# Optimization experiments

Hardware: AMD Instinct MI355X
Metric: run time of the kernel (lower is better)

The kernel has to match this reference:

```python
import jax, jax.numpy as jnp
import numpy as np

IN_CH = 256
SCALES = (128.0, 256.0, 512.0)
RATIOS = (0.5, 1.0, 2.0)
A = len(SCALES) * len(RATIOS)
PRE_NMS_TOPK = 2000
POST_NMS_TOPK = 1000
NMS_IOU = 0.7
MIN_SIZE = 16.0
RPN_BATCH = 256
POS_FRAC = 0.5
BBOX_CLAMP = float(np.log(1000.0 / 16.0))


def conv2d(x, w, b, pad):
    y = jax.lax.conv_general_dilated(x, w, (1, 1), [(pad, pad), (pad, pad)],
                                     dimension_numbers=('NCHW', 'OIHW', 'NCHW'))
    return y + b[None, :, None, None]


def generate_anchors(img_hw, feat_hw):
    H, W = img_hw
    Hf, Wf = feat_hw
    sh, sw = H // Hf, W // Wf
    r = jnp.asarray(RATIOS, jnp.float32)
    s = jnp.asarray(SCALES, jnp.float32)
    hr = jnp.sqrt(r)
    wr = 1.0 / hr
    ws = (wr[:, None] * s[None, :]).reshape(-1)  # [A]
    hs = (hr[:, None] * s[None, :]).reshape(-1)
    base = jnp.stack([-ws, -hs, ws, hs], axis=1) * 0.5  # [A,4] zero-centered
    xs = jnp.arange(Wf, dtype=jnp.float32) * sw
    ys = jnp.arange(Hf, dtype=jnp.float32) * sh
    yy, xx = jnp.meshgrid(ys, xs, indexing='ij')
    shifts = jnp.stack([xx, yy, xx, yy], axis=-1).reshape(-1, 4)  # [Hf*Wf,4]
    return (shifts[:, None, :] + base[None, :, :]).reshape(-1, 4)  # [Hf*Wf*A,4]


def apply_deltas(anchors, deltas):
    aw = anchors[:, 2] - anchors[:, 0]
    ah = anchors[:, 3] - anchors[:, 1]
    acx = anchors[:, 0] + 0.5 * aw
    acy = anchors[:, 1] + 0.5 * ah
    dx, dy = deltas[:, 0], deltas[:, 1]
    dw = jnp.minimum(deltas[:, 2], BBOX_CLAMP)
    dh = jnp.minimum(deltas[:, 3], BBOX_CLAMP)
    cx = dx * aw + acx
    cy = dy * ah + acy
    w = jnp.exp(dw) * aw
    h = jnp.exp(dh) * ah
    return jnp.stack([cx - 0.5 * w, cy - 0.5 * h, cx + 0.5 * w, cy + 0.5 * h], axis=1)


def boxes_to_deltas(boxes, anchors):
    aw = anchors[:, 2] - anchors[:, 0]
    ah = anchors[:, 3] - anchors[:, 1]
    acx = anchors[:, 0] + 0.5 * aw
    acy = anchors[:, 1] + 0.5 * ah
    gw = boxes[:, 2] - boxes[:, 0]
    gh = boxes[:, 3] - boxes[:, 1]
    gcx = boxes[:, 0] + 0.5 * gw
    gcy = boxes[:, 1] + 0.5 * gh
    return jnp.stack([(gcx - acx) / aw, (gcy - acy) / ah,
                      jnp.log(gw / aw), jnp.log(gh / ah)], axis=1)


def iou_matrix(a, b):
    area_a = (a[:, 2] - a[:, 0]) * (a[:, 3] - a[:, 1])
    area_b = (b[:, 2] - b[:, 0]) * (b[:, 3] - b[:, 1])
    lt = jnp.maximum(a[:, None, :2], b[None, :, :2])
    rb = jnp.minimum(a[:, None, 2:], b[None, :, 2:])
    wh = jnp.clip(rb - lt, 0.0)
    inter = wh[..., 0] * wh[..., 1]
    return inter / (area_a[:, None] + area_b[None, :] - inter)


def filter_proposals(proposals, logits):
    k = PRE_NMS_TOPK
    top_scores, idx = jax.lax.top_k(logits, k)
    boxes = proposals[idx]
    probs = jax.nn.sigmoid(top_scores)
    bw = boxes[:, 2] - boxes[:, 0]
    bh = boxes[:, 3] - boxes[:, 1]
    probs = jnp.where((bw >= MIN_SIZE) & (bh >= MIN_SIZE), probs, -jnp.inf)
    order = jnp.argsort(-probs)
    boxes = boxes[order]
    probs = probs[order]
    iou = iou_matrix(boxes, boxes)  # [k,k]
    idxs = jnp.arange(k)

    def body(i, keep):
        suppress = keep[i] & (iou[i] > NMS_IOU) & (idxs > i)
        return keep & ~suppress

    keep = jax.lax.fori_loop(0, k, body, jnp.ones(k, bool))
    kept = jnp.where(keep, probs, -jnp.inf)
    final_scores, fidx = jax.lax.top_k(kept, POST_NMS_TOPK)
    return boxes[fidx], final_scores


def _forward(image, feat_map, gt_boxes, w_rpn, b_rpn, w_reg, b_reg, w_cls, b_cls):
    img_hw = image.shape[-2:]
    feat_hw = feat_map.shape[-2:]
    conv_out = jax.nn.relu(conv2d(feat_map, w_rpn, b_rpn, 1))
    reg = conv2d(conv_out, w_reg, b_reg, 0).transpose(0, 2, 3, 1).reshape(-1, 4)
    cls = conv2d(conv_out, w_cls, b_cls, 0).transpose(0, 2, 3, 1).reshape(-1)
    anchors = generate_anchors(img_hw, feat_hw)  # [N,4]
    proposals = apply_deltas(anchors, jax.lax.stop_gradient(reg))
    H, W = img_hw
    proposals = jnp.stack([jnp.clip(proposals[:, 0], 0.0, W),
                           jnp.clip(proposals[:, 1], 0.0, H),
                           jnp.clip(proposals[:, 2], 0.0, W),
                           jnp.clip(proposals[:, 3], 0.0, H)], axis=1)
    prop_out, score_out = filter_proposals(proposals, jax.lax.stop_gradient(cls))

    # --- target assignment (training path) ---
    gt = gt_boxes[0]  # [M,4]
    iou = iou_matrix(anchors, gt)  # [N,M]
    max_iou = iou.max(axis=1)
    argmax_gt = iou.argmax(axis=1)
    labels = jnp.where(max_iou >= 0.7, 1.0, jnp.where(max_iou < 0.3, 0.0, -1.0))
    best_per_gt = iou.max(axis=0)  # [M]
    force_pos = (iou == best_per_gt[None, :]).any(axis=1)
    labels = jnp.where(force_pos, 1.0, labels)
    matched = gt[argmax_gt]
    tgt_deltas = boxes_to_deltas(matched, anchors)

    # --- deterministic positive/negative sampling (fixed key) ---
    N = labels.shape[0]
    u = jax.random.uniform(jax.random.key(42), (N,))
    pos_cap = int(POS_FRAC * RPN_BATCH)
    pv, pi = jax.lax.top_k(jnp.where(labels == 1.0, u, -jnp.inf), pos_cap)
    pos_valid = pv > -jnp.inf
    pos_mask = jnp.zeros(N, bool).at[pi].set(pos_valid)
    num_pos = pos_valid.sum()
    nv, ni = jax.lax.top_k(jnp.where(labels == 0.0, u, -jnp.inf), RPN_BATCH)
    neg_valid = (nv > -jnp.inf) & (jnp.arange(RPN_BATCH) < (RPN_BATCH - num_pos))
    neg_mask = jnp.zeros(N, bool).at[ni].set(neg_valid)
    samp_mask = pos_mask | neg_mask
    n_samp = samp_mask.sum().astype(jnp.float32)

    # BCE with logits (stable), mean over sampled anchors
    bce = jnp.maximum(cls, 0.0) - cls * labels + jnp.log1p(jnp.exp(-jnp.abs(cls)))
    cls_loss = jnp.sum(jnp.where(samp_mask, bce, 0.0)) / n_samp

    # smooth L1 (beta=1/9), sum over positives / num sampled
    beta = 1.0 / 9.0
    d = reg - tgt_deltas
    ad = jnp.abs(d)
    sl1 = jnp.where(ad < beta, 0.5 * d * d / beta, ad - 0.5 * beta)
    loc_loss = jnp.sum(jnp.where(pos_mask[:, None], sl1, 0.0)) / n_samp

    return prop_out, score_out, cls_loss, loc_loss


def setup_inputs() -> dict:
    key = jax.random.key(0)
    ks = jax.random.split(key, 8)
    image = jax.random.normal(ks[0], (1, 3, 800, 800), jnp.float32)
    feat_map = jax.random.normal(ks[1], (1, IN_CH, 100, 100), jnp.float32)
    cxy = jax.random.uniform(ks[2], (1, 20, 2), minval=100.0, maxval=700.0)
    wh = jax.random.uniform(ks[3], (1, 20, 2), minval=50.0, maxval=300.0)
    gt_boxes = jnp.concatenate([jnp.clip(cxy - 0.5 * wh, 0.0, 800.0),
                                jnp.clip(cxy + 0.5 * wh, 0.0, 800.0)], axis=-1)
    w_rpn = 0.01 * jax.random.normal(ks[4], (IN_CH, IN_CH, 3, 3), jnp.float32)
    b_rpn = jnp.zeros((IN_CH,), jnp.float32)
    w_reg = 0.01 * jax.random.normal(ks[5], (A * 4, IN_CH, 1, 1), jnp.float32)
    b_reg = jnp.zeros((A * 4,), jnp.float32)
    w_cls = 0.01 * jax.random.normal(ks[6], (A, IN_CH, 1, 1), jnp.float32)
    b_cls = jnp.zeros((A,), jnp.float32)
    return dict(image=image, feat_map=feat_map, gt_boxes=gt_boxes,
                w_rpn=w_rpn, b_rpn=b_rpn, w_reg=w_reg, b_reg=b_reg,
                w_cls=w_cls, b_cls=b_cls)


def reference(image, feat_map, gt_boxes, w_rpn, b_rpn, w_reg, b_reg, w_cls, b_cls):
    return _forward(image, feat_map, gt_boxes, w_rpn, b_rpn, w_reg, b_reg, w_cls, b_cls)
```

## Files before the change

### kernel.cpp

```cpp
#include <hip/hip_runtime.h>
#include <cstdint>
#include <cstddef>
#include <math.h>

typedef unsigned int u32;
typedef unsigned long long u64;
typedef unsigned char u8;
typedef signed char i8;
typedef unsigned short u16;

#define NPIX 10000
#define NANCH 90000
#define NGT 20
#define DIVUP(a,b) (((a)+(b)-1)/(b))

static constexpr float BBOX_CLAMP_F = 4.135166556742356f;
static constexpr float BETA_F       = 0.1111111111111111111f;
static constexpr float HALF_BETA_F  = 0.0555555555555555556f;

static constexpr size_t algn(size_t x){ return (x + 255) & ~size_t(255); }
static constexpr size_t OFF_WT   = 0;
static constexpr size_t OFF_W1T  = algn(OFF_WT   + size_t(2304)*256*4);
static constexpr size_t OFF_REG  = algn(OFF_W1T  + size_t(64*48*4)*4);
static constexpr size_t OFF_CLS  = algn(OFF_REG  + size_t(NANCH)*4*4);
static constexpr size_t OFF_PROP = algn(OFF_CLS  + size_t(NANCH)*4);
static constexpr size_t OFF_UB   = algn(OFF_PROP + size_t(NANCH)*4*4);
static constexpr size_t OFF_LAB  = algn(OFF_UB   + size_t(NANCH)*4);
static constexpr size_t OFF_AMX  = algn(OFF_LAB  + NANCH);
static constexpr size_t OFF_BGTP = algn(OFF_AMX  + NANCH);
static constexpr size_t OFF_BGT  = algn(OFF_BGTP + 1280*20*4);
static constexpr size_t OFF_BOXA = algn(OFF_BGT  + 256);
static constexpr size_t OFF_BOX2 = algn(OFF_BOXA + 2048*4*4);
static constexpr size_t OFF_PRB2 = algn(OFF_BOX2 + 2048*4*4);
static constexpr size_t OFF_SPRB = algn(OFF_PRB2 + 2048*4);
static constexpr size_t OFF_MASK = algn(OFF_SPRB + 2048*4);
static constexpr size_t OFF_CAND = algn(OFF_MASK + size_t(2048)*32*8);
static constexpr size_t OFF_CND2 = algn(OFF_CAND + 2048*8);
static constexpr size_t OFF_POSL = algn(OFF_CND2 + 4096*8);
static constexpr size_t OFF_EQN  = algn(OFF_POSL + 4096*4);
static constexpr size_t OFF_KEEP = algn(OFF_EQN  + 1024*8);
static constexpr size_t OFF_Z0   = algn(OFF_KEEP + 32*8);
static constexpr size_t OFF_H0   = OFF_Z0;
static constexpr size_t OFF_H2   = OFF_H0 + 65536*4;
static constexpr size_t OFF_META = OFF_H2 + 65536*4;
static constexpr size_t ZERO_END = OFF_META + 256;
static constexpr int ZERO_WORDS  = int((ZERO_END - OFF_Z0) / 4);

enum { M_CAND_CNT=0, M_POS_CNT, M_EQN_CNT, M_NEED_NEG,
       M_BIN_L_HI, M_CUM_L_HI, M_BIN_N_HI, M_CUM_N_HI,
       M_ACC_CLS, M_ACC_LOC, M_N_SAMP, M_CAND2_CNT };

__device__ __forceinline__ u32 rotl32(u32 x, int d){ return (x<<d)|(x>>(32-d)); }

__device__ __forceinline__ u32 threefry_bits(u32 i) {
  const u32 ks0 = 0u, ks1 = 42u, ks2 = 0x1BD11BDAu ^ 0u ^ 42u;
  u32 x0 = 0u + ks0, x1 = i + ks1;
  x0+=x1; x1=rotl32(x1,13); x1^=x0;
  x0+=x1; x1=rotl32(x1,15); x1^=x0;
  x0+=x1; x1=rotl32(x1,26); x1^=x0;
  x0+=x1; x1=rotl32(x1, 6); x1^=x0;
  x0+=ks1; x1+=ks2+1u;
  x0+=x1; x1=rotl32(x1,17); x1^=x0;
  x0+=x1; x1=rotl32(x1,29); x1^=x0;
  x0+=x1; x1=rotl32(x1,16); x1^=x0;
  x0+=x1; x1=rotl32(x1,24); x1^=x0;
  x0+=ks2; x1+=ks0+2u;
  x0+=x1; x1=rotl32(x1,13); x1^=x0;
  x0+=x1; x1=rotl32(x1,15); x1^=x0;
  x0+=x1; x1=rotl32(x1,26); x1^=x0;
  x0+=x1; x1=rotl32(x1, 6); x1^=x0;
  x0+=ks0; x1+=ks1+3u;
  x0+=x1; x1=rotl32(x1,17); x1^=x0;
  x0+=x1; x1=rotl32(x1,29); x1^=x0;
  x0+=x1; x1=rotl32(x1,16); x1^=x0;
  x0+=x1; x1=rotl32(x1,24); x1^=x0;
  x0+=ks1; x1+=ks2+4u;
  x0+=x1; x1=rotl32(x1,13); x1^=x0;
  x0+=x1; x1=rotl32(x1,15); x1^=x0;
  x0+=x1; x1=rotl32(x1,26); x1^=x0;
  x0+=x1; x1=rotl32(x1, 6); x1^=x0;
  x0+=ks2; x1+=ks0+5u;
  return x1;
}

__device__ __forceinline__ u32 rand_u_bits(u32 i) {
  u32 b = threefry_bits(i);
  float f = __uint_as_float((b >> 9) | 0x3F800000u) - 1.0f;
  return __float_as_uint(f);
}

__device__ __forceinline__ u32 fkey(float x) {
  u32 u = __float_as_uint(x);
  return (u & 0x80000000u) ? ~u : (u | 0x80000000u);
}

__device__ void bitonic_desc(u64* s, int N, int tid, int nthr) {
  for (int k = 2; k <= N; k <<= 1) {
    for (int j = k >> 1; j > 0; j >>= 1) {
      __syncthreads();
      for (int i = tid; i < N; i += nthr) {
        int ixj = i ^ j;
        if (ixj > i) {
          u64 a = s[i], b = s[ixj];
          bool up = ((i & k) == 0);
          if ((a < b) == up) { s[i] = b; s[ixj] = a; }
        }
      }
    }
  }
  __syncthreads();
}

__device__ __forceinline__ int wave_append(u32* cnt, bool pred) {
  u64 mb = __ballot(pred);
  if (mb == 0ull) return -1;
  int lane = threadIdx.x & 63;
  int leader = __ffsll((unsigned long long)mb) - 1;
  u32 base = 0;
  if (lane == leader) base = atomicAdd(cnt, (u32)__popcll(mb));
  base = __shfl(base, leader, 64);
  if (!pred) return -1;
  return (int)(base + (u32)__popcll(mb & ((1ull << lane) - 1ull)));
}

__device__ __forceinline__ u32 group_sum256(const u32* __restrict__ h, int g, int lane) {
  uint4 v = ((const uint4*)(h + (size_t)g*256))[lane];
  u32 s = v.x + v.y + v.z + v.w;
  #pragma unroll
  for (int off = 32; off > 0; off >>= 1) s += __shfl_down(s, off, 64);
  return s;
}

__global__ __launch_bounds__(256) void k_init(const float* __restrict__ w,
                                              const float* __restrict__ w_reg,
                                              const float* __restrict__ w_cls,
                                              float* __restrict__ wT,
                                              float* __restrict__ w1T,
                                              u32* __restrict__ zbase, int zwords) {
  int b = blockIdx.x;
  int t = threadIdx.x;
  if (b < 144) {
    __shared__ float sm[64][65];
    int ct = b / 36, et = b % 36;
    int e0 = et*64, co0 = ct*64;
    int lane = t & 63, rr = t >> 6;
    #pragma unroll
    for (int r4 = 0; r4 < 16; ++r4) {
      int row = r4*4 + rr;
      sm[row][lane] = w[(size_t)(co0+row)*2304 + e0 + lane];
    }
    __syncthreads();
    #pragma unroll
    for (int r4 = 0; r4 < 16; ++r4) {
      int erow = r4*4 + rr;
      wT[(size_t)(e0+erow)*256 + co0 + lane] = sm[lane][erow];
    }
  } else if (b == 144) {
    for (int i = t; i < 64*48*4; i += 256) {
      int e = i & 3, c = (i >> 2) % 48, g = (i >> 2) / 48;
      float v = 0.f;
      if (c < 36) v = w_reg[(size_t)c*256 + g*4 + e];
      else if (c < 45) v = w_cls[(size_t)(c-36)*256 + g*4 + e];
      w1T[i] = v;
    }
  } else {
    int nb = gridDim.x - 145;
    for (int i = (b-145)*256 + t; i < zwords; i += nb*256) zbase[i] = 0u;
  }
}

__device__ __forceinline__ float conv1_dot_t(const float4* __restrict__ f4,
                                             const float4* __restrict__ w1T4,
                                             int c, float bias) {
  float acc = bias;
  #pragma unroll 8
  for (int g = 0; g < 64; ++g) {
    float4 a = f4[g], b = w1T4[g*48 + c];
    acc += a.x*b.x + a.y*b.y + a.z*b.z + a.w*b.w;
  }
  return acc;
}

#pragma clang fp contract(off)

__device__ __forceinline__ void anchor_of(int n, float& a0, float& a1, float& a2, float& a3) {
  int px = n / 9, a = n % 9;
  int y = px / 100, x = px % 100;
  int ri = a / 3, si = a % 3;
  const float R[3] = {0.5f, 1.0f, 2.0f};
  const float S[3] = {128.f, 256.f, 512.f};
  float hr = sqrtf(R[ri]);
  float wr = 1.0f / hr;
  float wsa = wr * S[si], hsa = hr * S[si];
  float sx = (float)x * 8.0f, sy = (float)y * 8.0f;
  a0 = sx + (-wsa) * 0.5f;
  a1 = sy + (-hsa) * 0.5f;
  a2 = sx + wsa * 0.5f;
  a3 = sy + hsa * 0.5f;
}

__device__ __forceinline__ float iou_one(float a0,float a1,float a2,float a3,float aarea,
                                         const float* __restrict__ gt, int g) {
  float g0=gt[g*4+0], g1=gt[g*4+1], g2=gt[g*4+2], g3=gt[g*4+3];
  float garea=(g2-g0)*(g3-g1);
  float ix0=fmaxf(a0,g0), iy0=fmaxf(a1,g1);
  float ix1=fminf(a2,g2), iy1=fminf(a3,g3);
  float iw=fmaxf(ix1-ix0,0.f), ih=fmaxf(iy1-iy0,0.f);
  float inter=iw*ih;
  return inter/(aarea+garea-inter);
}

__device__ __forceinline__ float bce_of(float c, float l) {
  return fmaxf(c,0.f) - c*l + log1pf(expf(-fabsf(c)));
}

__global__ __launch_bounds__(256) void k_conv3(const float* __restrict__ feat,
                                               const float* __restrict__ wT,
                                               const float* __restrict__ bias,
                                               const float* __restrict__ w1T,
                                               const float* __restrict__ b_reg,
                                               const float* __restrict__ b_cls,
                                               const float* __restrict__ gt,
                                               float* __restrict__ reg,
                                               float* __restrict__ cls,
                                               float* __restrict__ prop,
                                               u32* __restrict__ h0,
                                               i8* __restrict__ label,
                                               u8* __restrict__ amax,
                                               u32* __restrict__ ub,
                                               float* __restrict__ bgtp) {
  const int co = threadIdx.x;
  const int y0 = (blockIdx.x / 25) * 2;
  const int x0 = (blockIdx.x % 25) * 4;
  __shared__ __align__(16) float sf[16][4][8];
  __shared__ __align__(16) float sacc[8][256];
  __shared__ float shead[8][48];
  __shared__ float sbias[48];
  __shared__ float sgt[80];
  __shared__ float svm[72][20];
  float acc[2][4];
  #pragma unroll
  for (int r = 0; r < 2; ++r)
    #pragma unroll
    for (int p = 0; p < 4; ++p) acc[r][p] = 0.f;

  for (int cb = 0; cb < 256; cb += 16) {
    __syncthreads();
    #pragma unroll
    for (int e = threadIdx.x; e < 512; e += 256) {
      int ci = e >> 5, rem = e & 31, r = rem >> 3, xx = rem & 7;
      int gy = y0 - 1 + r, gx = x0 - 1 + xx;
      float v = 0.f;
      if ((unsigned)gy < 100u && (unsigned)gx < 100u) v = feat[(cb+ci)*NPIX + gy*100 + gx];
      sf[ci][r][xx] = v;
    }
    __syncthreads();
    float wv0[9], wv1[9];
    {
      const float* wp = wT + (size_t)(cb*9)*256 + co;
      #pragma unroll
      for (int k = 0; k < 9; ++k) wv0[k] = wp[k*256];
    }
    #pragma unroll
    for (int ci = 0; ci < 16; ++ci) {
      float* cur = (ci & 1) ? wv1 : wv0;
      float* nxt = (ci & 1) ? wv0 : wv1;
      if (ci < 15) {
        const float* wp = wT + (size_t)((cb+ci+1)*9)*256 + co;
        #pragma unroll
        for (int k = 0; k < 9; ++k) nxt[k] = wp[k*256];
      }
      #pragma unroll
      for (int ir = 0; ir < 4; ++ir) {
        const float4* rp4 = (const float4*)&sf[ci][ir][0];
        float4 q0 = rp4[0], q1 = rp4[1];
        float rw[6] = {q0.x, q0.y, q0.z, q0.w, q1.x, q1.y};
        #pragma unroll
        for (int ky = 0; ky < 3; ++ky) {
          const int ro = ir - ky;
          if (ro >= 0 && ro < 2) {
            #pragma unroll
            for (int kx = 0; kx < 3; ++kx) {
              const float wvv = cur[ky*3+kx];
              #pragma unroll
              for (int p = 0; p < 4; ++p)
                acc[ro][p] = fmaf(wvv, rw[p+kx], acc[ro][p]);
            }
          }
        }
      }
    }
  }
  float b = bias[co];
  #pragma unroll
  for (int r = 0; r < 2; ++r)
    #pragma unroll
    for (int p = 0; p < 4; ++p)
      sacc[r*4+p][co] = fmaxf(acc[r][p] + b, 0.f);
  if (threadIdx.x < 45)
    sbias[threadIdx.x] = (threadIdx.x < 36) ? b_reg[threadIdx.x] : b_cls[threadIdx.x-36];
  if (threadIdx.x < 80) sgt[threadIdx.x] = gt[threadIdx.x];
  __syncthreads();
  for (int task = threadIdx.x; task < 360; task += 256) {
    int pl = task / 45, c = task % 45;
    float v = conv1_dot_t((const float4*)&sacc[pl][0], (const float4*)w1T, c, sbias[c]);
    shead[pl][c] = v;
    int px = (y0 + (pl >> 2))*100 + x0 + (pl & 3);
    if (c < 36) reg[(size_t)px*36 + c] = v;
    else        cls[(size_t)px*9 + (c-36)] = v;
  }
  __syncthreads();
  if (threadIdx.x < 72) {
    int pl = threadIdx.x / 9, aidx = threadIdx.x % 9;
    int px = (y0 + (pl >> 2))*100 + x0 + (pl & 3);
    int n = px*9 + aidx;
    float a0,a1,a2,a3; anchor_of(n, a0,a1,a2,a3);
    float aw = a2 - a0, ah = a3 - a1;
    float acx = a0 + 0.5f*aw, acy = a1 + 0.5f*ah;
    {
      float dx = shead[pl][aidx*4+0], dy = shead[pl][aidx*4+1];
      float dw = fminf(shead[pl][aidx*4+2], BBOX_CLAMP_F);
      float dh = fminf(shead[pl][aidx*4+3], BBOX_CLAMP_F);
      float lg = shead[pl][36+aidx];
      float cx = dx*aw + acx, cy = dy*ah + acy;
      float w = expf(dw)*aw, h = expf(dh)*ah;
      float p0 = cx - 0.5f*w, p1 = cy - 0.5f*h, p2 = cx + 0.5f*w, p3 = cy + 0.5f*h;
      p0 = fminf(fmaxf(p0, 0.f), 800.f);
      p1 = fminf(fmaxf(p1, 0.f), 800.f);
      p2 = fminf(fmaxf(p2, 0.f), 800.f);
      p3 = fminf(fmaxf(p3, 0.f), 800.f);
      prop[(size_t)n*4+0] = p0; prop[(size_t)n*4+1] = p1;
      prop[(size_t)n*4+2] = p2; prop[(size_t)n*4+3] = p3;
      atomicAdd(&h0[fkey(lg) >> 16], 1u);
    }
    float aarea = (a2-a0)*(a3-a1);
    float best = -1.f; int bg = 0;
    for (int g = 0; g < NGT; ++g) {
      float iou = iou_one(a0,a1,a2,a3,aarea,sgt,g);
      svm[threadIdx.x][g] = iou;
      if (iou > best) { best = iou; bg = g; }
    }
    label[n] = (best >= 0.7f) ? (i8)1 : ((best < 0.3f) ? (i8)0 : (i8)-1);
    amax[n] = (u8)bg;
    ub[n] = rand_u_bits((u32)n);
  }
  __syncthreads();
  if (threadIdx.x < NGT) {
    float m = 0.f;
    for (int r = 0; r < 72; ++r) m = fmaxf(m, svm[r][threadIdx.x]);
    bgtp[(size_t)blockIdx.x*NGT + threadIdx.x] = m;
  }
}

__global__ __launch_bounds__(1024) void k_scan(const u32* __restrict__ h0,
                                               const float* __restrict__ bgtp,
                                               u32* __restrict__ meta,
                                               float* __restrict__ bgt) {
  __shared__ u32 part[256], buf[256], sseg, scum;
  __shared__ float pb[32][20];
  int tid = threadIdx.x;
  int lane = tid & 63, wave = tid >> 6;
  for (int gi = 0; gi < 16; ++gi) {
    int g = wave*16 + gi;
    u32 s = group_sum256(h0, g, lane);
    if (lane == 0) part[g] = s;
  }
  if (tid < 640) {
    int g = tid % 20, ch = tid / 20;
    int r0 = ch*40, r1 = r0 + 40; if (r1 > 1250) r1 = 1250;
    float m = 0.f;
    for (int r = r0; r < r1; ++r) m = fmaxf(m, bgtp[(size_t)r*NGT + g]);
    pb[ch][g] = m;
  }
  __syncthreads();
  if (tid == 0) {
    u32 cum = 0; int seg = 255;
    for (; seg > 0; --seg) { if (cum + part[seg] >= 2000u) break; cum += part[seg]; }
    sseg = (u32)seg; scum = cum;
  }
  if (tid < 20) {
    float m = 0.f;
    #pragma unroll
    for (int c = 0; c < 32; ++c) m = fmaxf(m, pb[c][tid]);
    bgt[tid] = m;
  }
  __syncthreads();
  if (tid < 256) buf[tid] = h0[sseg*256 + tid];
  __syncthreads();
  if (tid == 0) {
    u32 cum = scum; int bin = (int)sseg*256;
    for (int i = 255; i >= 0; --i) {
      u32 h = buf[i];
      if (cum + h >= 2000u) { bin = (int)sseg*256 + i; break; }
      cum += h;
    }
    meta[M_BIN_L_HI] = (u32)bin;
  }
}

__global__ __launch_bounds__(256) void k_force(const float* __restrict__ cls,
                                               const float* __restrict__ bgt,
                                               const float* __restrict__ gt,
                                               i8* __restrict__ label,
                                               const u32* __restrict__ ub,
                                               u32* __restrict__ meta,
                                               u32* __restrict__ poslist,
                                               u32* __restrict__ h2,
                                               u64* __restrict__ cand,
                                               u64* __restrict__ cand2) {
  __shared__ float sgt[80], sbgt[20];
  int tid = threadIdx.x;
  if (tid < 80) sgt[tid] = gt[tid];
  if (tid < 20) sbgt[tid] = bgt[tid];
  __syncthreads();
  int n = blockIdx.x*256 + tid;
  bool valid = n < NANCH;
  u32 bin = meta[M_BIN_L_HI];
  bool pos = false, predA = false, predB = false; u64 ckey = 0;
  if (valid) {
    u32 k = fkey(cls[n]);
    u32 hi = k >> 16;
    if (hi >= bin) {
      ckey = ((u64)k << 32) | (u64)(0xFFFFFFFFu - (u32)n);
      if (hi > bin) predA = true; else predB = true;
    }
    float a0,a1,a2,a3; anchor_of(n, a0,a1,a2,a3);
    float aarea = (a2-a0)*(a3-a1);
    bool force = false;
    for (int g = 0; g < NGT; ++g)
      if (iou_one(a0,a1,a2,a3,aarea,sgt,g) == sbgt[g]) force = true;
    i8 lab = label[n];
    if (force) lab = 1;
    label[n] = lab;
    if (lab == 1) pos = true;
    else if (lab == 0) atomicAdd(&h2[ub[n] >> 16], 1u);
  }
  int slot = wave_append(&meta[M_POS_CNT], pos);
  if (pos && slot >= 0 && slot < 4096) poslist[slot] = (u32)n;
  int aslot = wave_append(&meta[M_CAND_CNT], predA);
  if (predA && aslot >= 0 && aslot < 2048) cand[aslot] = ckey;
  int bslot = wave_append(&meta[M_CAND2_CNT], predB);
  if (predB && bslot >= 0 && bslot < 4096) cand2[bslot] = ckey;
}

struct MidSh {
  union {
    struct { u64 ss[2048]; } srtA;
    struct { u64 ss[4096]; } srtB;
    struct { u32 part[256]; u32 buf[256]; } ns;
    struct { u64 ss[4096]; u32 sel[128]; float red[1024]; } ps;
  } u;
  u32 sseg, scum;
};

__device__ __forceinline__ void mid_gather(const u64* __restrict__ ss, int cnt, int base,
                                           const float* __restrict__ cls,
                                           const float* __restrict__ prop,
                                           float* __restrict__ boxA,
                                           float* __restrict__ sprobG,
                                           int tid) {
  for (int t = tid; t < cnt; t += 1024) {
    int rank = base + t;
    if (rank >= 2000) break;
    u32 n = 0xFFFFFFFFu - (u32)ss[t];
    float b0 = prop[(size_t)n*4+0], b1 = prop[(size_t)n*4+1];
    float b2 = prop[(size_t)n*4+2], b3 = prop[(size_t)n*4+3];
    float logit = cls[n];
    float p = 1.0f / (1.0f + expf(-logit));
    float bw = b2 - b0, bh = b3 - b1;
    if (!(bw >= 16.0f && bh >= 16.0f)) p = -INFINITY;
    boxA[rank*4+0] = b0; boxA[rank*4+1] = b1; boxA[rank*4+2] = b2; boxA[rank*4+3] = b3;
    sprobG[rank] = p;
  }
}

__global__ __launch_bounds__(1024) void k_mid(const u64* __restrict__ cand,
                                              const u64* __restrict__ cand2,
                                              const float* __restrict__ cls,
                                              const float* __restrict__ prop,
                                              const float* __restrict__ reg,
                                              const float* __restrict__ gt,
                                              const u32* __restrict__ ub,
                                              const u32* __restrict__ poslist,
                                              const u8* __restrict__ amax,
                                              const u32* __restrict__ h2,
                                              u32* __restrict__ meta,
                                              float* __restrict__ boxA,
                                              float* __restrict__ sprobG) {
  __shared__ MidSh S;
  int tid = threadIdx.x;
  int lane = tid & 63, wave = tid >> 6;
  if (blockIdx.x == 0) {
    u32 c1 = meta[M_CAND_CNT]; if (c1 > 2048u) c1 = 2048u;
    if (c1 > 0) {
      int N = 256; while (N < (int)c1) N <<= 1;
      for (int i = tid; i < N; i += 1024) S.u.srtA.ss[i] = (i < (int)c1) ? cand[i] : 0ull;
      bitonic_desc(S.u.srtA.ss, N, tid, 1024);
      mid_gather(S.u.srtA.ss, (int)c1, 0, cls, prop, boxA, sprobG, tid);
    }
  } else if (blockIdx.x == 3) {
    u32 c1 = meta[M_CAND_CNT]; if (c1 > 2048u) c1 = 2048u;
    u32 c2 = meta[M_CAND2_CNT]; if (c2 > 4096u) c2 = 4096u;
    int lim = 2000 - (int)c1; if (lim < 0) lim = 0; if (lim > (int)c2) lim = (int)c2;
    if (c2 > 0 && lim > 0) {
      int N = 256; while (N < (int)c2) N <<= 1;
      for (int i = tid; i < N; i += 1024) S.u.srtB.ss[i] = (i < (int)c2) ? cand2[i] : 0ull;
      bitonic_desc(S.u.srtB.ss, N, tid, 1024);
      mid_gather(S.u.srtB.ss, lim, (int)c1, cls, prop, boxA, sprobG, tid);
    }
  } else if (blockIdx.x == 1) {
    u32 pc = meta[M_POS_CNT]; if (pc > 4096u) pc = 4096u;
    int npos = pc < 128u ? (int)pc : 128;
    u32 need = (u32)(256 - npos);
    if (tid == 0) meta[M_NEED_NEG] = need;
    for (int gi = 0; gi < 16; ++gi) {
      int g = wave*16 + gi;
      u32 s = group_sum256(h2, g, lane);
      if (lane == 0) S.u.ns.part[g] = s;
    }
    __syncthreads();
    if (tid == 0) {
      u32 cum = 0; int seg = 255;
      for (; seg > 0; --seg) { if (cum + S.u.ns.part[seg] >= need) break; cum += S.u.ns.part[seg]; }
      S.sseg = (u32)seg; S.scum = cum;
    }
    __syncthreads();
    if (tid < 256) S.u.ns.buf[tid] = h2[S.sseg*256 + tid];
    __syncthreads();
    if (tid == 0) {
      u32 cum = S.scum; int bin = (int)S.sseg*256;
      for (int i = 255; i >= 0; --i) {
        u32 h = S.u.ns.buf[i];
        if (cum + h >= need) { bin = (int)S.sseg*256 + i; break; }
        cum += h;
      }
      meta[M_BIN_N_HI] = (u32)bin;
      meta[M_CUM_N_HI] = cum;
    }
  } else {
    u32 m = meta[M_POS_CNT]; if (m > 4096u) m = 4096u;
    int npos = m < 128u ? (int)m : 128;
    if (m > 128u) {
      int N = 256; while (N < (int)m) N <<= 1;
      for (int i = tid; i < N; i += 1024)
        S.u.ps.ss[i] = (i < (int)m)
          ? (((u64)ub[poslist[i]] << 32) | (u64)(0xFFFFFFFFu - poslist[i]))
          : 0ull;
      bitonic_desc(S.u.ps.ss, N, tid, 1024);
      if (tid < 128) S.u.ps.sel[tid] = 0xFFFFFFFFu - (u32)S.u.ps.ss[tid];
    } else {
      if (tid < (int)m) S.u.ps.sel[tid] = poslist[tid];
    }
    __syncthreads();
    float accC = 0.f, accL = 0.f;
    if (tid < npos) {
      int n = (int)S.u.ps.sel[tid];
      float c = cls[n];
      accC = bce_of(c, 1.0f);
      float a0,a1,a2,a3; anchor_of(n, a0,a1,a2,a3);
      float aw = a2-a0, ah = a3-a1;
      float acx = a0 + 0.5f*aw, acy = a1 + 0.5f*ah;
      int g = amax[n];
      float g0 = gt[g*4+0], g1 = gt[g*4+1], g2 = gt[g*4+2], g3 = gt[g*4+3];
      float gw = g2-g0, gh = g3-g1;
      float gcx = g0 + 0.5f*gw, gcy = g1 + 0.5f*gh;
      float t0 = (gcx-acx)/aw, t1 = (gcy-acy)/ah;
      float t2 = logf(gw/aw), t3 = logf(gh/ah);
      float tt[4] = {t0,t1,t2,t3};
      float sl = 0.f;
      for (int j = 0; j < 4; ++j) {
        float d = reg[(size_t)n*4 + j] - tt[j];
        float ad = fabsf(d);
        sl += (ad < BETA_F) ? (((0.5f*d)*d)/BETA_F) : (ad - HALF_BETA_F);
      }
      accL = sl;
    }
    __syncthreads();
    S.u.ps.red[tid] = accC;
    __syncthreads();
    for (int s = 512; s > 0; s >>= 1) {
      if (tid < s) S.u.ps.red[tid] = S.u.ps.red[tid] + S.u.ps.red[tid+s];
      __syncthreads();
    }
    float totC = S.u.ps.red[0];
    __syncthreads();
    S.u.ps.red[tid] = accL;
    __syncthreads();
    for (int s = 512; s > 0; s >>= 1) {
      if (tid < s) S.u.ps.red[tid] = S.u.ps.red[tid] + S.u.ps.red[tid+s];
      __syncthreads();
    }
    if (tid == 0) {
      float* mf = (float*)meta;
      atomicAdd(&mf[M_ACC_CLS], totC);
      atomicAdd(&mf[M_ACC_LOC], S.u.ps.red[0]);
      atomicAdd(&meta[M_N_SAMP], (u32)npos);
    }
  }
}

struct NnSh {
  union {
    struct { float bx0[2000], by0[2000], bx1[2000], by1[2000], bar[2000], sp[2000];
             u16 dmap[2000]; } nms;
    struct { float redf[1024]; u32 redc[1024]; } neg;
  } u;
};

__global__ __launch_bounds__(1024) void k_nn(const float* __restrict__ boxA,
                                             const float* __restrict__ sprobG,
                                             const float* __restrict__ cls,
                                             const i8* __restrict__ label,
                                             const u32* __restrict__ ub,
                                             u32* __restrict__ meta,
                                             u64* __restrict__ eqn,
                                             u64* __restrict__ mask,
                                             float* __restrict__ box2k,
                                             float* __restrict__ prob2k) {
  __shared__ NnSh S;
  int tid = threadIdx.x;
  int lane = tid & 63;
  int wave = tid >> 6;
  if (blockIdx.x < 125) {
    for (int i = tid; i < 2000; i += 1024) {
      float x0 = boxA[i*4+0], y0 = boxA[i*4+1], x1 = boxA[i*4+2], y1 = boxA[i*4+3];
      S.u.nms.bx0[i]=x0; S.u.nms.by0[i]=y0; S.u.nms.bx1[i]=x1; S.u.nms.by1[i]=y1;
      S.u.nms.bar[i] = (x1-x0)*(y1-y0);
      S.u.nms.sp[i] = sprobG[i];
    }
    __syncthreads();
    if (wave == 0) {
      u32 nkeep = 0;
      for (int c = 0; c < 32; ++c) {
        int i = c*64 + lane;
        bool k = (i < 2000) && (S.u.nms.sp[i] > -INFINITY);
        nkeep += (u32)__popcll(__ballot(k));
      }
      u32 rk = 0, rf = 0;
      for (int c = 0; c < 32; ++c) {
        int i = c*64 + lane;
        bool inb = (i < 2000);
        bool k = inb && (S.u.nms.sp[i] > -INFINITY);
        u64 mk = __ballot(k);
        u64 mf = __ballot(inb && !k);
        if (inb) {
          u64 below = (1ull << lane) - 1ull;
          u32 dst = k ? (rk + (u32)__popcll(mk & below))
                      : (nkeep + rf + (u32)__popcll(mf & below));
          S.u.nms.dmap[dst] = (u16)i;
        }
        rk += (u32)__popcll(mk);
        rf += (u32)__popcll(mf);
      }
    }
    __syncthreads();
    if (blockIdx.x == 0) {
      for (int t = tid; t < 2000; t += 1024) {
        u32 s = S.u.nms.dmap[t];
        prob2k[t] = S.u.nms.sp[s];
        box2k[t*4+0] = S.u.nms.bx0[s]; box2k[t*4+1] = S.u.nms.by0[s];
        box2k[t*4+2] = S.u.nms.bx1[s]; box2k[t*4+3] = S.u.nms.by1[s];
      }
    }
    int i = blockIdx.x*16 + wave;
    if (i < 2000) {
      u32 di = S.u.nms.dmap[i];
      float x0 = S.u.nms.bx0[di], y0 = S.u.nms.by0[di];
      float x1 = S.u.nms.bx1[di], y1 = S.u.nms.by1[di];
      float ai = S.u.nms.bar[di];
      #pragma unroll 4
      for (int w = 0; w < 32; ++w) {
        int j = w*64 + lane;
        bool sup = false;
        if (j < 2000 && j > i) {
          u32 dj = S.u.nms.dmap[j];
          float ix0 = fmaxf(x0, S.u.nms.bx0[dj]), iy0 = fmaxf(y0, S.u.nms.by0[dj]);
          float ix1 = fminf(x1, S.u.nms.bx1[dj]), iy1 = fminf(y1, S.u.nms.by1[dj]);
          float iw = fmaxf(ix1-ix0, 0.f), ih = fmaxf(iy1-iy0, 0.f);
          float inter = iw*ih;
          float iou = inter / (ai + S.u.nms.bar[dj] - inter);
          sup = iou > 0.7f;
        }
        u64 m = __ballot(sup);
        if (lane == 0) mask[(size_t)i*32 + w] = m;
      }
    }
  } else {
    u32 binN = meta[M_BIN_N_HI];
    int n = (blockIdx.x - 125)*1024 + tid;
    float accC = 0.f; u32 cnt = 0;
    bool inbin = false; u64 key = 0;
    if (n < NANCH && label[n] == 0) {
      u32 u = ub[n];
      u32 hi = u >> 16;
      if (hi > binN) { accC = bce_of(cls[n], 0.0f); cnt = 1; }
      else if (hi == binN) { inbin = true; key = ((u64)(u & 0xFFFFu) << 32) | (u64)(0xFFFFFFFFu - (u32)n); }
    }
    int slot = wave_append(&meta[M_EQN_CNT], inbin);
    if (inbin && slot >= 0 && slot < 1024) eqn[slot] = key;
    S.u.neg.redf[tid] = accC; S.u.neg.redc[tid] = cnt;
    __syncthreads();
    for (int s = 512; s > 0; s >>= 1) {
      if (tid < s) { S.u.neg.redf[tid] = S.u.neg.redf[tid] + S.u.neg.redf[tid+s];
                     S.u.neg.redc[tid] += S.u.neg.redc[tid+s]; }
      __syncthreads();
    }
    if (tid == 0 && (S.u.neg.redc[0] > 0 || S.u.neg.redf[0] != 0.f)) {
      float* mf = (float*)meta;
      atomicAdd(&mf[M_ACC_CLS], S.u.neg.redf[0]);
      atomicAdd(&meta[M_N_SAMP], S.u.neg.redc[0]);
    }
  }
}

__global__ __launch_bounds__(1024) void k_final(const float* __restrict__ cls,
                                                const u64* __restrict__ eqn,
                                                const u64* __restrict__ mask,
                                                const float* __restrict__ box2k,
                                                const float* __restrict__ prob2k,
                                                u32* __restrict__ meta,
                                                u64* __restrict__ keep,
                                                float* __restrict__ out) {
  __shared__ union {
    u64 ss[1024];
    struct { u32 kw32[64]; u64 keptw; u32 rc[64][64]; } nsc;
    struct { u16 srcmap[1000]; int ngood; } fin;
  } sh;
  __shared__ float red[1024];
  int tid = threadIdx.x;
  int lane = tid & 63, wave = tid >> 6;
  u32 m = meta[M_EQN_CNT]; if (m > 1024u) m = 1024u;
  int N2 = 128; while (N2 < (int)m) N2 <<= 1;
  if (tid < N2) sh.ss[tid] = (tid < (int)m) ? eqn[tid] : 0ull;
  bitonic_desc(sh.ss, N2, tid, 1024);
  int ntake = (int)meta[M_NEED_NEG] - (int)meta[M_CUM_N_HI];
  if (ntake < 0) ntake = 0;
  if (ntake > (int)m) ntake = (int)m;
  float accC = 0.f;
  if (tid < ntake) {
    u32 n = 0xFFFFFFFFu - (u32)sh.ss[tid];
    accC = bce_of(cls[n], 0.0f);
  }
  red[tid] = accC;
  __syncthreads();
  for (int s = 512; s > 0; s >>= 1) {
    if (tid < s) red[tid] = red[tid] + red[tid+s];
    __syncthreads();
  }
  if (tid == 0) {
    float* mf = (float*)meta;
    mf[M_ACC_CLS] = mf[M_ACC_CLS] + red[0];
    meta[M_N_SAMP] = meta[M_N_SAMP] + (u32)ntake;
  }
  __syncthreads();
  {
    const u32* mask32 = (const u32*)mask;
    if (tid < 64) sh.nsc.kw32[tid] = (tid < 62) ? 0xFFFFFFFFu : (tid == 62 ? 0xFFFFu : 0u);
    __syncthreads();
    for (int widx = 0; widx < 32; ++widx) {
      for (int e = tid; e < 4096; e += 1024) {
        int r = e >> 6, w = e & 63;
        int i = widx*64 + r;
        sh.nsc.rc[r][w] = (i < 2000) ? mask32[(size_t)i*64 + w] : 0u;
      }
      __syncthreads();
      if (wave == 0) {
        u64 dj = (u64)sh.nsc.rc[lane][2*widx] | ((u64)sh.nsc.rc[lane][2*widx+1] << 32);
        u64 alive = ((u64)sh.nsc.kw32[widx*2+1] << 32) | (u64)sh.nsc.kw32[widx*2];
        u64 todo = alive;
        while (todo) {
          int b = __builtin_ctzll(todo);
          u64 supp = __shfl(dj, b, 64);
          alive &= ~supp;
          u64 below = (b == 63) ? ~0ull : ((1ull << (b+1)) - 1ull);
          todo = alive & ~below;
        }
        if (lane == 0) {
          sh.nsc.kw32[widx*2]   = (u32)alive;
          sh.nsc.kw32[widx*2+1] = (u32)(alive >> 32);
          sh.nsc.keptw = alive;
        }
      }
      __syncthreads();
      u64 t = sh.nsc.keptw;
      int rank = 0;
      while (t) {
        int b = __builtin_ctzll(t);
        t &= t - 1;
        if ((rank & 15) == wave) {
          u32 mm = sh.nsc.rc[b][lane];
          if (mm) atomicAnd(&sh.nsc.kw32[lane], ~mm);
        }
        ++rank;
      }
      __syncthreads();
    }
    if (tid < 32) keep[tid] = ((u64)sh.nsc.kw32[tid*2+1] << 32) | (u64)sh.nsc.kw32[tid*2];
  }
  __syncthreads();
  if (tid < 64) {
    int base = 0;
    for (int c = 0; c < 32; ++c) {
      int i = c*64 + lane;
      bool good = false;
      if (i < 2000) good = (((keep[i>>6] >> (i&63)) & 1ull) != 0) && (prob2k[i] > -INFINITY);
      u64 mb = __ballot(good);
      if (good) {
        int r = base + (int)__popcll(mb & ((1ull << lane) - 1ull));
        if (r < 1000) sh.fin.srcmap[r] = (u16)i;
      }
      base += (int)__popcll(mb);
    }
    int ng = base < 1000 ? base : 1000;
    if (lane == 0) sh.fin.ngood = ng;
    int fill = ng;
    for (int c = 0; c < 32 && fill < 1000; ++c) {
      int i = c*64 + lane;
      bool bad = false;
      if (i < 2000) bad = !((((keep[i>>6] >> (i&63)) & 1ull) != 0) && (prob2k[i] > -INFINITY));
      u64 mb = __ballot(bad);
      if (bad) {
        int r = fill + (int)__popcll(mb & ((1ull << lane) - 1ull));
        if (r < 1000) sh.fin.srcmap[r] = (u16)i;
      }
      fill += (int)__popcll(mb);
    }
  }
  __syncthreads();
  int ng = sh.fin.ngood;
  for (int s = tid; s < 1000; s += 1024) {
    int src = sh.fin.srcmap[s];
    out[4000 + s] = (s < ng) ? prob2k[src] : -3.0e38f;
    out[s*4+0] = box2k[src*4+0];
    out[s*4+1] = box2k[src*4+1];
    out[s*4+2] = box2k[src*4+2];
    out[s*4+3] = box2k[src*4+3];
  }
  if (tid == 0) {
    const float* mf = (const float*)meta;
    u32 nsv = meta[M_N_SAMP];
    float nsamp = (nsv > 0u) ? (float)nsv : 1.0f;
    out[5000] = mf[M_ACC_CLS] / nsamp;
    out[5001] = mf[M_ACC_LOC] / nsamp;
  }
}

extern "C" void kernel_launch(void* const* d_in, const int* in_sizes, int n_in,
                              void* d_out, int out_size, void* d_ws, size_t ws_size,
                              hipStream_t stream) {
  const float* feat  = (const float*)d_in[1];
  const float* gt    = (const float*)d_in[2];
  const float* w_rpn = (const float*)d_in[3];
  const float* b_rpn = (const float*)d_in[4];
  const float* w_reg = (const float*)d_in[5];
  const float* b_reg = (const float*)d_in[6];
  const float* w_cls = (const float*)d_in[7];
  const float* b_cls = (const float*)d_in[8];
  float* out = (float*)d_out;
  char* ws = (char*)d_ws;

  float* wT     = (float*)(ws + OFF_WT);
  float* w1T    = (float*)(ws + OFF_W1T);
  float* reg    = (float*)(ws + OFF_REG);
  float* cls    = (float*)(ws + OFF_CLS);
  float* prop   = (float*)(ws + OFF_PROP);
  u32*   ub     = (u32*)  (ws + OFF_UB);
  i8*    label  = (i8*)   (ws + OFF_LAB);
  u8*    amax   = (u8*)   (ws + OFF_AMX);
  float* bgtp   = (float*)(ws + OFF_BGTP);
  float* bgt    = (float*)(ws + OFF_BGT);
  float* boxA   = (float*)(ws + OFF_BOXA);
  float* box2k  = (float*)(ws + OFF_BOX2);
  float* prob2k = (float*)(ws + OFF_PRB2);
  float* sprobG = (float*)(ws + OFF_SPRB);
  u64*   mask   = (u64*)  (ws + OFF_MASK);
  u64*   cand   = (u64*)  (ws + OFF_CAND);
  u64*   cand2  = (u64*)  (ws + OFF_CND2);
  u32*   poslist= (u32*)  (ws + OFF_POSL);
  u64*   eqn    = (u64*)  (ws + OFF_EQN);
  u64*   keep   = (u64*)  (ws + OFF_KEEP);
  u32*   h0     = (u32*)  (ws + OFF_H0);
  u32*   h2     = (u32*)  (ws + OFF_H2);
  u32*   meta   = (u32*)  (ws + OFF_META);

  k_init<<<145 + 64, 256, 0, stream>>>(w_rpn, w_reg, w_cls, wT, w1T,
                                       (u32*)(ws + OFF_Z0), ZERO_WORDS);
  k_conv3<<<1250, 256, 0, stream>>>(feat, wT, b_rpn, w1T, b_reg, b_cls, gt,
                                    reg, cls, prop, h0, label, amax, ub, bgtp);
  k_scan<<<1, 1024, 0, stream>>>(h0, bgtp, meta, bgt);
  k_force<<<DIVUP(NANCH,256), 256, 0, stream>>>(cls, bgt, gt, label, ub, meta,
                                                poslist, h2, cand, cand2);
  k_mid<<<4, 1024, 0, stream>>>(cand, cand2, cls, prop, reg, gt, ub, poslist,
                                amax, h2, meta, boxA, sprobG);
  k_nn<<<125 + DIVUP(NANCH,1024), 1024, 0, stream>>>(boxA, sprobG, cls, label,
                                                     ub, meta, eqn, mask,
                                                     box2k, prob2k);
  k_final<<<1, 1024, 0, stream>>>(cls, eqn, mask, box2k, prob2k, meta, keep, out);
}
```

Baseline: 593.0 us.

## Move negative histogram into conv, double-buffer NMS mask rows, split conv launch

The negative-label histogram is now built in the conv kernel, and the force kernel only decrements it for anchors that are promoted to positive. The best-IoU-per-GT reduction in the scan kernel becomes a shared-memory atomicMax over float bits. The final NMS loop double-buffers the mask rows so the other waves prefetch the next 64-row chunk while wave 0 resolves the current one, which removes one barrier per iteration. The conv kernel is also launched as two half-grids with a block offset. This adds an extra launch and more atomics in exchange.

```diff
diff --git a/kernel.cpp b/kernel.cpp
--- a/kernel.cpp
+++ b/kernel.cpp
@@ -225,13 +225,16 @@
                                                float* __restrict__ cls,
                                                float* __restrict__ prop,
                                                u32* __restrict__ h0,
+                                               u32* __restrict__ h2,
                                                i8* __restrict__ label,
                                                u8* __restrict__ amax,
                                                u32* __restrict__ ub,
-                                               float* __restrict__ bgtp) {
+                                               float* __restrict__ bgtp,
+                                               int boff) {
   const int co = threadIdx.x;
-  const int y0 = (blockIdx.x / 25) * 2;
-  const int x0 = (blockIdx.x % 25) * 4;
+  const int bid = blockIdx.x + boff;
+  const int y0 = (bid / 25) * 2;
+  const int x0 = (bid % 25) * 4;
   __shared__ __align__(16) float sf[16][4][8];
   __shared__ __align__(16) float sacc[8][256];
   __shared__ float shead[8][48];
@@ -340,15 +343,18 @@
       svm[threadIdx.x][g] = iou;
       if (iou > best) { best = iou; bg = g; }
     }
-    label[n] = (best >= 0.7f) ? (i8)1 : ((best < 0.3f) ? (i8)0 : (i8)-1);
+    i8 lab = (best >= 0.7f) ? (i8)1 : ((best < 0.3f) ? (i8)0 : (i8)-1);
+    label[n] = lab;
     amax[n] = (u8)bg;
-    ub[n] = rand_u_bits((u32)n);
+    u32 u = rand_u_bits((u32)n);
+    ub[n] = u;
+    if (lab == 0) atomicAdd(&h2[u >> 16], 1u);
   }
   __syncthreads();
   if (threadIdx.x < NGT) {
     float m = 0.f;
     for (int r = 0; r < 72; ++r) m = fmaxf(m, svm[r][threadIdx.x]);
-    bgtp[(size_t)blockIdx.x*NGT + threadIdx.x] = m;
+    bgtp[(size_t)bid*NGT + threadIdx.x] = m;
   }
 }
 
@@ -357,34 +363,25 @@
                                                u32* __restrict__ meta,
                                                float* __restrict__ bgt) {
   __shared__ u32 part[256], buf[256], sseg, scum;
-  __shared__ float pb[32][20];
+  __shared__ u32 sbgtu[20];
   int tid = threadIdx.x;
   int lane = tid & 63, wave = tid >> 6;
+  if (tid < 20) sbgtu[tid] = 0u;
   for (int gi = 0; gi < 16; ++gi) {
     int g = wave*16 + gi;
     u32 s = group_sum256(h0, g, lane);
     if (lane == 0) part[g] = s;
   }
-  if (tid < 640) {
-    int g = tid % 20, ch = tid / 20;
-    int r0 = ch*40, r1 = r0 + 40; if (r1 > 1250) r1 = 1250;
-    float m = 0.f;
-    for (int r = r0; r < r1; ++r) m = fmaxf(m, bgtp[(size_t)r*NGT + g]);
-    pb[ch][g] = m;
-  }
-  __syncthreads();
+  __syncthreads();
+  for (int e = tid; e < 1250*NGT; e += 1024)
+    atomicMax(&sbgtu[e % NGT], __float_as_uint(bgtp[e]));
   if (tid == 0) {
     u32 cum = 0; int seg = 255;
     for (; seg > 0; --seg) { if (cum + part[seg] >= 2000u) break; cum += part[seg]; }
     sseg = (u32)seg; scum = cum;
   }
-  if (tid < 20) {
-    float m = 0.f;
-    #pragma unroll
-    for (int c = 0; c < 32; ++c) m = fmaxf(m, pb[c][tid]);
-    bgt[tid] = m;
-  }
-  __syncthreads();
+  __syncthreads();
+  if (tid < 20) bgt[tid] = __uint_as_float(sbgtu[tid]);
   if (tid < 256) buf[tid] = h0[sseg*256 + tid];
   __syncthreads();
   if (tid == 0) {
@@ -430,10 +427,12 @@
     for (int g = 0; g < NGT; ++g)
       if (iou_one(a0,a1,a2,a3,aarea,sgt,g) == sbgt[g]) force = true;
     i8 lab = label[n];
-    if (force) lab = 1;
-    label[n] = lab;
+    if (force && lab != 1) {
+      if (lab == 0) atomicSub(&h2[ub[n] >> 16], 1u);
+      label[n] = (i8)1;
+      lab = 1;
+    }
     if (lab == 1) pos = true;
-    else if (lab == 0) atomicAdd(&h2[ub[n] >> 16], 1u);
   }
   int slot = wave_append(&meta[M_POS_CNT], pos);
   if (pos && slot >= 0 && slot < 4096) poslist[slot] = (u32)n;
@@ -723,7 +722,7 @@
                                                 float* __restrict__ out) {
   __shared__ union {
     u64 ss[1024];
-    struct { u32 kw32[64]; u64 keptw; u32 rc[64][64]; } nsc;
+    struct { u32 kw32[64]; u64 keptw; u32 rc[2][64][64]; } nsc;
     struct { u16 srcmap[1000]; int ngood; } fin;
   } sh;
   __shared__ float red[1024];
@@ -756,16 +755,15 @@
   {
     const u32* mask32 = (const u32*)mask;
     if (tid < 64) sh.nsc.kw32[tid] = (tid < 62) ? 0xFFFFFFFFu : (tid == 62 ? 0xFFFFu : 0u);
+    for (int e = tid; e < 4096; e += 1024) {
+      int r = e >> 6, w = e & 63;
+      sh.nsc.rc[0][r][w] = (r < 2000) ? mask32[(size_t)r*64 + w] : 0u;
+    }
     __syncthreads();
     for (int widx = 0; widx < 32; ++widx) {
-      for (int e = tid; e < 4096; e += 1024) {
-        int r = e >> 6, w = e & 63;
-        int i = widx*64 + r;
-        sh.nsc.rc[r][w] = (i < 2000) ? mask32[(size_t)i*64 + w] : 0u;
-      }
-      __syncthreads();
+      const int cur = widx & 1;
       if (wave == 0) {
-        u64 dj = (u64)sh.nsc.rc[lane][2*widx] | ((u64)sh.nsc.rc[lane][2*widx+1] << 32);
+        u64 dj = (u64)sh.nsc.rc[cur][lane][2*widx] | ((u64)sh.nsc.rc[cur][lane][2*widx+1] << 32);
         u64 alive = ((u64)sh.nsc.kw32[widx*2+1] << 32) | (u64)sh.nsc.kw32[widx*2];
         u64 todo = alive;
         while (todo) {
@@ -780,6 +778,12 @@
           sh.nsc.kw32[widx*2+1] = (u32)(alive >> 32);
           sh.nsc.keptw = alive;
         }
+      } else if (widx < 31) {
+        for (int e = tid - 64; e < 4096; e += 960) {
+          int r = e >> 6, w = e & 63;
+          int i = (widx+1)*64 + r;
+          sh.nsc.rc[cur^1][r][w] = (i < 2000) ? mask32[(size_t)i*64 + w] : 0u;
+        }
       }
       __syncthreads();
       u64 t = sh.nsc.keptw;
@@ -788,7 +792,7 @@
         int b = __builtin_ctzll(t);
         t &= t - 1;
         if ((rank & 15) == wave) {
-          u32 mm = sh.nsc.rc[b][lane];
+          u32 mm = sh.nsc.rc[cur][b][lane];
           if (mm) atomicAnd(&sh.nsc.kw32[lane], ~mm);
         }
         ++rank;
@@ -885,8 +889,10 @@
 
   k_init<<<145 + 64, 256, 0, stream>>>(w_rpn, w_reg, w_cls, wT, w1T,
                                        (u32*)(ws + OFF_Z0), ZERO_WORDS);
-  k_conv3<<<1250, 256, 0, stream>>>(feat, wT, b_rpn, w1T, b_reg, b_cls, gt,
-                                    reg, cls, prop, h0, label, amax, ub, bgtp);
+  k_conv3<<<625, 256, 0, stream>>>(feat, wT, b_rpn, w1T, b_reg, b_cls, gt,
+                                   reg, cls, prop, h0, h2, label, amax, ub, bgtp, 0);
+  k_conv3<<<625, 256, 0, stream>>>(feat, wT, b_rpn, w1T, b_reg, b_cls, gt,
+                                   reg, cls, prop, h0, h2, label, amax, ub, bgtp, 625);
   k_scan<<<1, 1024, 0, stream>>>(h0, bgtp, meta, bgt);
   k_force<<<DIVUP(NANCH,256), 256, 0, stream>>>(cls, bgt, gt, label, ub, meta,
                                                 poslist, h2, cand, cand2);
```

New measurement: 596.3 us. Within noise of the previous version (+0.6%).
